# Kernel tuning notes

Measured on AMD Instinct MI355X. Metric: run time of the kernel, lower is better.

Reference implementation:

```python
import jax, jax.numpy as jnp
import numpy as np

N, B, FD, D, MSG, SCN, H, FFN = 2048, 16, 128, 32, 32, 16, 4, 64
HD = D // H


def _lin(k, o, i, scale=0.05):
    kw, kb = jax.random.split(k)
    return (jax.random.normal(kw, (o, i), jnp.float32) * scale,
            jax.random.normal(kb, (o,), jnp.float32) * scale)


def setup_inputs() -> dict:
    key = jax.random.key(0)
    ks = jax.random.split(key, 24)
    inp = {}
    inp['src'] = jax.random.randint(ks[0], (B,), 0, N)
    inp['dst'] = jax.random.randint(ks[1], (B,), 0, N)
    inp['edge_feat'] = jax.random.normal(ks[2], (B, 3), jnp.float32)
    inp['timestamps'] = jax.random.uniform(ks[3], (B,), dtype=jnp.float32)
    inp['node_features'] = jax.random.normal(ks[4], (N, FD), jnp.float32)
    inp['adj'] = jnp.zeros((N, N), jnp.float32)  # unused: assume_identity_adj=True
    inp['memory'] = jax.random.normal(ks[5], (N, D), jnp.float32) * 0.1
    inp['W_emb'], inp['b_emb'] = _lin(ks[6], D, FD)
    inp['Wqkv'], inp['bqkv'] = _lin(ks[7], 3 * D, D)
    inp['Wo'], inp['bo'] = _lin(ks[8], D, D)
    inp['g1'] = jnp.ones((D,), jnp.float32); inp['be1'] = jnp.zeros((D,), jnp.float32)
    inp['g2'] = jnp.ones((D,), jnp.float32); inp['be2'] = jnp.zeros((D,), jnp.float32)
    inp['W_f1'], inp['b_f1'] = _lin(ks[9], FFN, D)
    inp['W_f2'], inp['b_f2'] = _lin(ks[10], D, FFN)
    inp['W_scn'], inp['b_scn'] = _lin(ks[11], SCN, D)
    inp['g_scn'] = jnp.ones((SCN,), jnp.float32); inp['be_scn'] = jnp.zeros((SCN,), jnp.float32)
    inp['W_e1'], inp['b_e1'] = _lin(ks[12], 32, 2 * SCN)
    inp['W_e2'], inp['b_e2'] = _lin(ks[13], 16, 32)
    inp['W_e3'], inp['b_e3'] = _lin(ks[14], 1, 16)
    inp['gru_Wih'], inp['gru_bih'] = _lin(ks[15], 3 * D, MSG)
    inp['gru_Whh'], inp['gru_bhh'] = _lin(ks[16], 3 * D, D)
    inp['W_m1'], inp['b_m1'] = _lin(ks[17], MSG, 2 * D + 3)
    inp['W_m2'], inp['b_m2'] = _lin(ks[18], MSG, MSG)
    return inp


def _ln(x, g, b):
    mu = x.mean(-1, keepdims=True)
    var = ((x - mu) ** 2).mean(-1, keepdims=True)
    return (x - mu) * jax.lax.rsqrt(var + 1e-5) * g + b


def _gru(x, h, Wih, Whh, bih, bhh):
    # torch.nn.GRUCell semantics
    gi = x @ Wih.T + bih
    gh = h @ Whh.T + bhh
    ir, iz, i_n = jnp.split(gi, 3, -1)
    hr, hz, h_n = jnp.split(gh, 3, -1)
    r = jax.nn.sigmoid(ir + hr)
    z = jax.nn.sigmoid(iz + hz)
    n = jnp.tanh(i_n + r * h_n)
    return (1.0 - z) * n + z * h


def _update_memory(memory, src, dst, edge_feat,
                   gru_Wih, gru_Whh, gru_bih, gru_bhh, W_m1, b_m1, W_m2, b_m2):
    # messages computed from pre-update memory (as in torch source)
    msg_in = jnp.concatenate([memory[src], memory[dst], edge_feat], axis=1)  # [B, 2D+3]
    messages = jax.nn.relu(msg_in @ W_m1.T + b_m1) @ W_m2.T + b_m2           # [B, MSG]

    def step(mem, inp):
        s, d, m = inp
        hs = _gru(m, mem[s], gru_Wih, gru_Whh, gru_bih, gru_bhh)
        mem = mem.at[s].set(hs)
        hd = _gru(m, mem[d], gru_Wih, gru_Whh, gru_bih, gru_bhh)  # sees updated mem if d==s earlier
        mem = mem.at[d].set(hd)
        return mem, None

    new_mem, _ = jax.lax.scan(step, memory, (src, dst, messages))
    return new_mem


def _edge_logits(node_features, src, dst,
                 W_emb, b_emb, Wqkv, bqkv, Wo, bo, g1, be1, g2, be2,
                 W_f1, b_f1, W_f2, b_f2, W_scn, b_scn, g_scn, be_scn,
                 W_e1, b_e1, W_e2, b_e2, W_e3, b_e3):
    x0 = node_features @ W_emb.T + b_emb                      # [N, D]
    x = jnp.broadcast_to(x0[None], (B, N, D))                 # [B, N, D]
    # --- Graph transformer layer (MHA, eval mode: dropout = identity) ---
    qkv = x @ Wqkv.T + bqkv                                   # [B, N, 3D]
    q, k, v = jnp.split(qkv, 3, -1)
    q = q.reshape(B, N, H, HD)
    k = k.reshape(B, N, H, HD)
    v = v.reshape(B, N, H, HD)
    scores = jnp.einsum('bqhd,bkhd->bhqk', q, k) / np.sqrt(HD)
    attn = jax.nn.softmax(scores, axis=-1)
    ao = jnp.einsum('bhqk,bkhd->bqhd', attn, v).reshape(B, N, D)
    ao = ao @ Wo.T + bo
    x = _ln(x + ao, g1, be1)
    ffn = jax.nn.gelu(x @ W_f1.T + b_f1, approximate=False) @ W_f2.T + b_f2
    x = _ln(x + ffn, g2, be2)
    # --- SCN layer (identity adjacency assumed) ---
    s_out = jax.nn.relu(_ln(x @ W_scn.T + b_scn, g_scn, be_scn))  # [B, N, SCN]
    bi = jnp.arange(B)
    src_emb = s_out[bi, src]
    dst_emb = s_out[bi, dst]
    h = jnp.concatenate([src_emb, dst_emb], axis=-1)
    h = jax.nn.relu(h @ W_e1.T + b_e1)
    h = jax.nn.relu(h @ W_e2.T + b_e2)
    return (h @ W_e3.T + b_e3).squeeze(-1)                    # [B]


def reference(src, dst, edge_feat, timestamps, node_features, adj, memory,
              W_emb, b_emb, Wqkv, bqkv, Wo, bo, g1, be1, g2, be2,
              W_f1, b_f1, W_f2, b_f2, W_scn, b_scn, g_scn, be_scn,
              W_e1, b_e1, W_e2, b_e2, W_e3, b_e3,
              gru_Wih, gru_bih, gru_Whh, gru_bhh, W_m1, b_m1, W_m2, b_m2):
    new_mem = _update_memory(memory, src, dst, edge_feat,
                             gru_Wih, gru_Whh, gru_bih, gru_bhh,
                             W_m1, b_m1, W_m2, b_m2)
    edge_logit = _edge_logits(node_features, src, dst,
                              W_emb, b_emb, Wqkv, bqkv, Wo, bo, g1, be1, g2, be2,
                              W_f1, b_f1, W_f2, b_f2, W_scn, b_scn, g_scn, be_scn,
                              W_e1, b_e1, W_e2, b_e2, W_e3, b_e3)
    return edge_logit, new_mem
```

## Files before the change

kernel.cpp:

```cpp
#include <hip/hip_runtime.h>
#include <math.h>

#define NN   2048
#define BB   16

#define WS_X0   0
#define WS_QT   65536
#define WS_KT   131072
#define WS_VT   196608
#define WS_PART 262144
#define WS_GI   268800

__device__ __forceinline__ float sigmoidf_(float x) { return 1.0f / (1.0f + __expf(-x)); }
__device__ __forceinline__ float tanhf_(float x) {
    float ex = __expf(2.0f * x);
    return 1.0f - 2.0f / (ex + 1.0f);
}
__device__ __forceinline__ float dot4_(float4 a, float4 b) {
    return a.x*b.x + a.y*b.y + a.z*b.z + a.w*b.w;
}

__global__ __launch_bounds__(256) void k1_embed_qkv(
    const float* __restrict__ nf, const float* __restrict__ Wemb, const float* __restrict__ bemb,
    const float* __restrict__ Wqkv, const float* __restrict__ bqkv,
    const float* __restrict__ mem, const int* __restrict__ src, const int* __restrict__ dst,
    const float* __restrict__ ef,
    const float* __restrict__ Wm1, const float* __restrict__ bm1,
    const float* __restrict__ Wm2, const float* __restrict__ bm2,
    const float* __restrict__ Wih, const float* __restrict__ bih,
    float* __restrict__ ws, float* __restrict__ out)
{
    __shared__ float We_s[32 * 130];
    __shared__ float nf_s[8 * 130];
    __shared__ float x0_s[8 * 33];
    __shared__ float Wq_s[96 * 33];
    __shared__ __align__(16) float Wm1_s[32 * 67];
    __shared__ float Wm2_s[32 * 33];
    __shared__ float Wih_s[96 * 33];
    __shared__ float min_s[16 * 67];
    __shared__ float mr_s[16 * 33];
    __shared__ float msg_s[16 * 33];

    const int t = threadIdx.x, bx = blockIdx.x;

    if (bx == 256) {
        for (int idx = t; idx < 536; idx += 256)
            ((float4*)Wm1_s)[idx] = ((const float4*)Wm1)[idx];
        for (int idx = t; idx < 256; idx += 256) {
            float4 v = ((const float4*)Wm2)[idx];
            int o = idx >> 3, i = (idx & 7) * 4;
            Wm2_s[o * 33 + i] = v.x; Wm2_s[o * 33 + i + 1] = v.y;
            Wm2_s[o * 33 + i + 2] = v.z; Wm2_s[o * 33 + i + 3] = v.w;
        }
        for (int idx = t; idx < 768; idx += 256) {
            float4 v = ((const float4*)Wih)[idx];
            int o = idx >> 3, i = (idx & 7) * 4;
            Wih_s[o * 33 + i] = v.x; Wih_s[o * 33 + i + 1] = v.y;
            Wih_s[o * 33 + i + 2] = v.z; Wih_s[o * 33 + i + 3] = v.w;
        }
        for (int idx = t; idx < 16 * 67; idx += 256) {
            int e = idx / 67, i = idx - e * 67;
            float v;
            if (i < 32)      v = mem[src[e] * 32 + i];
            else if (i < 64) v = mem[dst[e] * 32 + (i - 32)];
            else             v = ef[e * 3 + (i - 64)];
            min_s[idx] = v;
        }
        __syncthreads();
        {
            int o = t & 31, e0 = t >> 5;
            for (int p = 0; p < 2; ++p) {
                int e = e0 + p * 8;
                float acc = bm1[o];
                for (int i = 0; i < 67; ++i) acc += Wm1_s[o * 67 + i] * min_s[e * 67 + i];
                mr_s[e * 33 + o] = fmaxf(acc, 0.f);
            }
        }
        __syncthreads();
        {
            int o = t & 31, e0 = t >> 5;
            for (int p = 0; p < 2; ++p) {
                int e = e0 + p * 8;
                float acc = bm2[o];
                #pragma unroll 8
                for (int i = 0; i < 32; ++i) acc += Wm2_s[o * 33 + i] * mr_s[e * 33 + i];
                msg_s[e * 33 + o] = acc;
            }
        }
        __syncthreads();
        {
            float* gi_g = ws + WS_GI;
            for (int idx = t; idx < 1536; idx += 256) {
                int e = idx / 96, o = idx - e * 96;
                float acc = bih[o];
                #pragma unroll 8
                for (int i = 0; i < 32; ++i) acc += Wih_s[o * 33 + i] * msg_s[e * 33 + i];
                gi_g[idx] = acc;
            }
        }
        return;
    }

    if (bx < 64) {
        int g = bx * 256 + t;
        ((float4*)(out + 16))[g] = ((const float4*)mem)[g];
    }

    const int j = t >> 5, o = t & 31;
    const int n = bx * 8 + j;

    for (int idx = t; idx < 1024; idx += 256) {
        float4 v = ((const float4*)Wemb)[idx];
        int r = idx >> 5, c = (idx & 31) * 4;
        We_s[r * 130 + c] = v.x; We_s[r * 130 + c + 1] = v.y;
        We_s[r * 130 + c + 2] = v.z; We_s[r * 130 + c + 3] = v.w;
    }
    for (int idx = t; idx < 768; idx += 256) {
        float4 v = ((const float4*)Wqkv)[idx];
        int r = idx >> 3, c = (idx & 7) * 4;
        Wq_s[r * 33 + c] = v.x; Wq_s[r * 33 + c + 1] = v.y;
        Wq_s[r * 33 + c + 2] = v.z; Wq_s[r * 33 + c + 3] = v.w;
    }
    for (int idx = t; idx < 256; idx += 256) {
        float4 v = ((const float4*)nf)[(bx * 8 + (idx >> 5)) * 32 + (idx & 31)];
        int r = idx >> 5, c = (idx & 31) * 4;
        nf_s[r * 130 + c] = v.x; nf_s[r * 130 + c + 1] = v.y;
        nf_s[r * 130 + c + 2] = v.z; nf_s[r * 130 + c + 3] = v.w;
    }
    __syncthreads();

    float acc = bemb[o];
    {
        const float2* Wr = (const float2*)&We_s[o * 130];
        const float2* Nr = (const float2*)&nf_s[j * 130];
        float sx = 0.f, sy = 0.f;
        #pragma unroll 16
        for (int i = 0; i < 64; ++i) {
            float2 w = Wr[i], x = Nr[i];
            sx += w.x * x.x; sy += w.y * x.y;
        }
        acc += sx + sy;
    }
    x0_s[j * 33 + o] = acc;
    ws[WS_X0 + n * 32 + o] = acc;
    __syncthreads();

    #pragma unroll
    for (int c = 0; c < 3; ++c) {
        int oo = c * 32 + o;
        float a2 = bqkv[oo];
        #pragma unroll 8
        for (int i = 0; i < 32; ++i) a2 += Wq_s[oo * 33 + i] * x0_s[j * 33 + i];
        int h = o >> 3, d = o & 7;
        float* base = ws + (c == 0 ? WS_QT : (c == 1 ? WS_KT : WS_VT));
        base[h * 16384 + n * 8 + d] = a2;
    }
}

__global__ __launch_bounds__(256) void k2_attn(
    const int* __restrict__ src, const int* __restrict__ dst,
    float* __restrict__ ws)
{
    const int t = threadIdx.x, bx = blockIdx.x;
    const int s  = bx >> 2;
    const int ks = bx & 3;
    const int h  = t >> 6;
    const int l  = t & 63;

    const int e = s >> 1;
    const int n = (s & 1) ? dst[e] : src[e];

    const float* qg = ws + WS_QT + h * 16384 + n * 8;
    const float4 qa  = *(const float4*)qg;
    const float4 qb4 = *(const float4*)(qg + 4);
    const float* kbase = ws + WS_KT + h * 16384;
    const float* vbase = ws + WS_VT + h * 16384;

    float4 oa = make_float4(0.f, 0.f, 0.f, 0.f);
    float4 ob = make_float4(0.f, 0.f, 0.f, 0.f);
    float ssum = 0.f;
    const float scale = 0.35355339059327373f;

    #pragma unroll
    for (int i = 0; i < 8; ++i) {
        const int key = ks * 512 + i * 64 + l;
        const float4 ka = *(const float4*)(kbase + key * 8);
        const float4 kb = *(const float4*)(kbase + key * 8 + 4);
        const float sc = (dot4_(qa, ka) + dot4_(qb4, kb)) * scale;
        const float p = __expf(sc);
        ssum += p;
        const float4 va = *(const float4*)(vbase + key * 8);
        const float4 vb = *(const float4*)(vbase + key * 8 + 4);
        oa.x += p * va.x; oa.y += p * va.y; oa.z += p * va.z; oa.w += p * va.w;
        ob.x += p * vb.x; ob.y += p * vb.y; ob.z += p * vb.z; ob.w += p * vb.w;
    }

    #pragma unroll
    for (int m = 1; m <= 32; m <<= 1) {
        ssum += __shfl_xor(ssum, m);
        oa.x += __shfl_xor(oa.x, m); oa.y += __shfl_xor(oa.y, m);
        oa.z += __shfl_xor(oa.z, m); oa.w += __shfl_xor(oa.w, m);
        ob.x += __shfl_xor(ob.x, m); ob.y += __shfl_xor(ob.y, m);
        ob.z += __shfl_xor(ob.z, m); ob.w += __shfl_xor(ob.w, m);
    }
    if (l == 0) {
        float* p = ws + WS_PART + ((s * 4 + h) * 4 + ks) * 12;
        *(float4*)p       = oa;
        *(float4*)(p + 4) = ob;
        p[8] = ssum;
    }
}

__global__ __launch_bounds__(1024) void k34_post_scan(
    const int* __restrict__ src, const int* __restrict__ dst,
    const float* __restrict__ mem,
    const float* __restrict__ Wo, const float* __restrict__ bo,
    const float* __restrict__ g1, const float* __restrict__ be1,
    const float* __restrict__ Wf1, const float* __restrict__ bf1,
    const float* __restrict__ Wf2, const float* __restrict__ bf2,
    const float* __restrict__ g2, const float* __restrict__ be2,
    const float* __restrict__ Wscn, const float* __restrict__ bscn,
    const float* __restrict__ gscn, const float* __restrict__ bescn,
    const float* __restrict__ Whh, const float* __restrict__ bhh,
    const float* __restrict__ We1, const float* __restrict__ be1e,
    const float* __restrict__ We2, const float* __restrict__ be2e,
    const float* __restrict__ We3, const float* __restrict__ be3,
    float* __restrict__ ws, float* __restrict__ out)
{
    __shared__ float Wo_s[32 * 33];
    __shared__ float Wf1_s[64 * 33];
    __shared__ float Wf2_s[32 * 65];
    __shared__ float Ws_s[16 * 33];
    __shared__ float arow[32 * 33];
    __shared__ float x1s[32 * 33];
    __shared__ float fs[32 * 65];
    __shared__ float sout_s[32 * 17];
    __shared__ float We1_s[32 * 33];
    __shared__ float We2_s[16 * 33];
    __shared__ float gi_s[16 * 97];
    __shared__ __align__(16) float slots[32 * 36];
    __shared__ int nid_s[32], fid_s[32], last_s[32];

    const int t = threadIdx.x;
    const int j = t >> 5, o = t & 31;

    float4 w1[8], w2[8], w3[8];
    float b1 = 0.f, b2 = 0.f, b3 = 0.f;
    if (t < 64) {
        const int r2 = (t < 32) ? t + 64 : t - 32;
        const int r3 = t + 32;
        #pragma unroll
        for (int c = 0; c < 8; ++c) {
            w1[c] = ((const float4*)Whh)[t * 8 + c];
            w2[c] = ((const float4*)Whh)[r2 * 8 + c];
            w3[c] = ((const float4*)Whh)[r3 * 8 + c];
        }
        b1 = bhh[t]; b2 = bhh[r2]; b3 = bhh[r3];
    }

    for (int idx = t; idx < 1024; idx += 1024) { int r = idx >> 5, c = idx & 31; Wo_s[r * 33 + c] = Wo[idx]; }
    for (int idx = t; idx < 2048; idx += 1024) { int r = idx >> 5, c = idx & 31; Wf1_s[r * 33 + c] = Wf1[idx]; }
    for (int idx = t; idx < 2048; idx += 1024) { int r = idx >> 6, c = idx & 63; Wf2_s[r * 65 + c] = Wf2[idx]; }
    for (int idx = t; idx < 512;  idx += 1024) { int r = idx >> 5, c = idx & 31; Ws_s[r * 33 + c] = Wscn[idx]; }
    for (int idx = t; idx < 1024; idx += 1024) { int r = idx >> 5, c = idx & 31; We1_s[r * 33 + c] = We1[idx]; }
    for (int idx = t; idx < 512;  idx += 1024) { int r = idx >> 5, c = idx & 31; We2_s[r * 33 + c] = We2[idx]; }
    for (int idx = t; idx < 1536; idx += 1024) { int e = idx / 96, oo = idx - e * 96; gi_s[e * 97 + oo] = ws[WS_GI + idx]; }
    if (t < 32) nid_s[t] = (t & 1) ? dst[t >> 1] : src[t >> 1];

    const int ej = j >> 1;
    const int n = (j & 1) ? dst[ej] : src[ej];
    {
        const int h = o >> 3, d = o & 7;
        float num = 0.f, den = 0.f;
        #pragma unroll
        for (int ks = 0; ks < 4; ++ks) {
            const float* p = ws + WS_PART + ((j * 4 + h) * 4 + ks) * 12;
            num += p[d];
            den += p[8];
        }
        arow[j * 33 + o] = num / den;
    }
    const float x0v = ws[WS_X0 + n * 32 + o];
    __syncthreads();

    if (t < 32) {
        int me = nid_s[t], f = t;
        for (int j2 = 0; j2 < t; ++j2) if (nid_s[j2] == me) { f = j2; break; }
        fid_s[t] = f;
        int isl = 1;
        for (int j2 = t + 1; j2 < 32; ++j2) if (nid_s[j2] == me) { isl = 0; break; }
        last_s[t] = isl;
    }
    float a = bo[o];
    #pragma unroll 8
    for (int i = 0; i < 32; ++i) a += Wo_s[o * 33 + i] * arow[j * 33 + i];
    float t1 = x0v + a;
    float mu = t1;
    #pragma unroll
    for (int m = 16; m >= 1; m >>= 1) mu += __shfl_xor(mu, m, 32);
    mu *= (1.f / 32.f);
    float dv = t1 - mu;
    float var = dv * dv;
    #pragma unroll
    for (int m = 16; m >= 1; m >>= 1) var += __shfl_xor(var, m, 32);
    var *= (1.f / 32.f);
    float x1 = dv * rsqrtf(var + 1e-5f) * g1[o] + be1[o];
    x1s[j * 33 + o] = x1;
    __syncthreads();

    if (t < 1024) {
        int j2 = t >> 5;
        if (fid_s[j2] == j2) slots[j2 * 36 + o] = mem[nid_s[j2] * 32 + o];
    }
    #pragma unroll
    for (int c = 0; c < 2; ++c) {
        int oo = c * 32 + o;
        float f = bf1[oo];
        #pragma unroll 8
        for (int i = 0; i < 32; ++i) f += Wf1_s[oo * 33 + i] * x1s[j * 33 + i];
        fs[j * 65 + oo] = 0.5f * f * (1.f + erff(f * 0.70710678118654752f));
    }
    __syncthreads();

    float f2 = bf2[o];
    #pragma unroll 8
    for (int i = 0; i < 64; ++i) f2 += Wf2_s[o * 65 + i] * fs[j * 65 + i];
    float t2 = x1 + f2;
    float mu2 = t2;
    #pragma unroll
    for (int m = 16; m >= 1; m >>= 1) mu2 += __shfl_xor(mu2, m, 32);
    mu2 *= (1.f / 32.f);
    float dv2 = t2 - mu2;
    float var2 = dv2 * dv2;
    #pragma unroll
    for (int m = 16; m >= 1; m >>= 1) var2 += __shfl_xor(var2, m, 32);
    var2 *= (1.f / 32.f);
    float x2 = dv2 * rsqrtf(var2 + 1e-5f) * g2[o] + be2[o];
    __syncthreads();
    x1s[j * 33 + o] = x2;
    __syncthreads();

    if (o < 16) {
        float sc = bscn[o];
        #pragma unroll 8
        for (int i = 0; i < 32; ++i) sc += Ws_s[o * 33 + i] * x1s[j * 33 + i];
        float m16 = sc;
        #pragma unroll
        for (int m = 8; m >= 1; m >>= 1) m16 += __shfl_xor(m16, m, 16);
        m16 *= (1.f / 16.f);
        float d16 = sc - m16;
        float v16 = d16 * d16;
        #pragma unroll
        for (int m = 8; m >= 1; m >>= 1) v16 += __shfl_xor(v16, m, 16);
        v16 *= (1.f / 16.f);
        float sv = d16 * rsqrtf(v16 + 1e-5f) * gscn[o] + bescn[o];
        sout_s[j * 17 + o] = fmaxf(sv, 0.f);
    }
    __syncthreads();

    if (t < 512) {
        int e = t >> 5, i = t & 31;
        arow[e * 33 + i] = (i < 16) ? sout_s[(2 * e) * 17 + i]
                                    : sout_s[(2 * e + 1) * 17 + (i - 16)];
    }
    __syncthreads();

    if (t < 512) {
        int e = t >> 5;
        float acc = be1e[o];
        #pragma unroll 8
        for (int i = 0; i < 32; ++i) acc += We1_s[o * 33 + i] * arow[e * 33 + i];
        fs[e * 33 + o] = fmaxf(acc, 0.f);
    }
    __syncthreads();

    if (t < 256) {
        int e = t >> 4, o2 = t & 15;
        float acc = be2e[o2];
        #pragma unroll 8
        for (int i = 0; i < 32; ++i) acc += We2_s[o2 * 33 + i] * fs[e * 33 + i];
        fs[600 + e * 17 + o2] = fmaxf(acc, 0.f);
    }
    __syncthreads();

    if (t < 16) {
        float acc = be3[0];
        #pragma unroll
        for (int i = 0; i < 16; ++i) acc += We3[i] * fs[600 + t * 17 + i];
        out[t] = acc;
    }
    __syncthreads();

    if (t < 64) {
        const bool lowhalf = (t < 32);
        for (int e = 0; e < 16; ++e) {
            const int js = 2 * e, jd = 2 * e + 1;
            const int ss = fid_s[js], sd = fid_s[jd];
            const bool same = (nid_s[js] == nid_s[jd]);
            const int npass = same ? 2 : 1;
            for (int pass = 0; pass < npass; ++pass) {
                const bool do_src = (!same) || (pass == 0);
                const bool do_dst = (!same) || (pass == 1);
                float acc1 = b1, acc2 = b2, acc3 = b3;
                #pragma unroll
                for (int c = 0; c < 8; ++c) {
                    const float4 hs4 = *(const float4*)&slots[ss * 36 + 4 * c];
                    const float4 hd4 = *(const float4*)&slots[sd * 36 + 4 * c];
                    acc1 += dot4_(w1[c], hs4);
                    const float4 hm = lowhalf ? hs4 : hd4;
                    acc2 += dot4_(w2[c], hm);
                    acc3 += dot4_(w3[c], hd4);
                }
                const float shv = __shfl_xor(lowhalf ? acc3 : acc1, 32);
                const float hr = lowhalf ? acc1 : acc2;
                const float hz = shv;
                const float hn = lowhalf ? acc2 : acc3;
                const float ir  = gi_s[e * 97 + o];
                const float iz  = gi_s[e * 97 + 32 + o];
                const float inn = gi_s[e * 97 + 64 + o];
                const float r = sigmoidf_(ir + hr);
                const float z = sigmoidf_(iz + hz);
                const float nn = tanhf_(inn + r * hn);
                const int slot = lowhalf ? ss : sd;
                const float hold = slots[slot * 36 + o];
                const float hnew = (1.f - z) * nn + z * hold;
                const bool wr = lowhalf ? do_src : do_dst;
                if (wr) slots[slot * 36 + o] = hnew;
                __threadfence_block();
            }
        }
    }
    __syncthreads();

    {
        int j2 = t >> 5;
        if (t < 1024 && last_s[j2]) out[16 + nid_s[j2] * 32 + o] = slots[fid_s[j2] * 36 + o];
    }
}

extern "C" void kernel_launch(void* const* d_in, const int* in_sizes, int n_in,
                              void* d_out, int out_size, void* d_ws, size_t ws_size,
                              hipStream_t stream)
{
    (void)in_sizes; (void)n_in; (void)out_size; (void)ws_size;
    const int*   src   = (const int*)d_in[0];
    const int*   dst   = (const int*)d_in[1];
    const float* ef    = (const float*)d_in[2];
    const float* nf    = (const float*)d_in[4];
    const float* mem   = (const float*)d_in[6];
    const float* Wemb  = (const float*)d_in[7];
    const float* bemb  = (const float*)d_in[8];
    const float* Wqkv  = (const float*)d_in[9];
    const float* bqkv  = (const float*)d_in[10];
    const float* Wo    = (const float*)d_in[11];
    const float* bo    = (const float*)d_in[12];
    const float* g1    = (const float*)d_in[13];
    const float* be1   = (const float*)d_in[14];
    const float* g2    = (const float*)d_in[15];
    const float* be2   = (const float*)d_in[16];
    const float* Wf1   = (const float*)d_in[17];
    const float* bf1   = (const float*)d_in[18];
    const float* Wf2   = (const float*)d_in[19];
    const float* bf2   = (const float*)d_in[20];
    const float* Wscn  = (const float*)d_in[21];
    const float* bscn  = (const float*)d_in[22];
    const float* gscn  = (const float*)d_in[23];
    const float* bescn = (const float*)d_in[24];
    const float* We1   = (const float*)d_in[25];
    const float* be1e  = (const float*)d_in[26];
    const float* We2   = (const float*)d_in[27];
    const float* be2e  = (const float*)d_in[28];
    const float* We3   = (const float*)d_in[29];
    const float* be3   = (const float*)d_in[30];
    const float* Wih   = (const float*)d_in[31];
    const float* bih   = (const float*)d_in[32];
    const float* Whh   = (const float*)d_in[33];
    const float* bhh   = (const float*)d_in[34];
    const float* Wm1   = (const float*)d_in[35];
    const float* bm1   = (const float*)d_in[36];
    const float* Wm2   = (const float*)d_in[37];
    const float* bm2   = (const float*)d_in[38];
    float* out = (float*)d_out;
    float* ws  = (float*)d_ws;

    hipLaunchKernelGGL(k1_embed_qkv, dim3(257), dim3(256), 0, stream,
        nf, Wemb, bemb, Wqkv, bqkv, mem, src, dst, ef, Wm1, bm1, Wm2, bm2, Wih, bih, ws, out);
    hipLaunchKernelGGL(k2_attn, dim3(128), dim3(256), 0, stream, src, dst, ws);
    hipLaunchKernelGGL(k34_post_scan, dim3(1), dim3(1024), 0, stream,
        src, dst, mem, Wo, bo, g1, be1, Wf1, bf1, Wf2, bf2, g2, be2,
        Wscn, bscn, gscn, bescn, Whh, bhh, We1, be1e, We2, be2e, We3, be3, ws, out);
}
```

Measured before the change: 203.2 us.

## Shrink post-scan block to 256 threads and batch weight loads into registers

The single-block post-scan kernel now runs with 256 threads instead of 1024. Each thread handles four rows through unrolled loops, and the weight staging now issues all vectorized global loads into registers up front before writing them to shared memory. The embed/QKV kernel and the memory-message block also prefetch their weights into registers before the shared-memory stores, so load latencies overlap. Going to fewer threads cuts barrier cost and wave count in the serial tail kernel, but each thread does more sequential work and uses more registers.

```diff
diff --git a/kernel.cpp b/kernel.cpp
--- a/kernel.cpp
+++ b/kernel.cpp
@@ -44,27 +44,46 @@
     const int t = threadIdx.x, bx = blockIdx.x;
 
     if (bx == 256) {
-        for (int idx = t; idx < 536; idx += 256)
-            ((float4*)Wm1_s)[idx] = ((const float4*)Wm1)[idx];
-        for (int idx = t; idx < 256; idx += 256) {
-            float4 v = ((const float4*)Wm2)[idx];
+        float4 rm1[3], rm2, rih[3];
+        float rmin[5];
+        #pragma unroll
+        for (int k = 0; k < 3; ++k) {
+            int idx = t + 256 * k;
+            rm1[k] = (idx < 536) ? ((const float4*)Wm1)[idx] : make_float4(0,0,0,0);
+        }
+        rm2 = ((const float4*)Wm2)[t];
+        #pragma unroll
+        for (int k = 0; k < 3; ++k) rih[k] = ((const float4*)Wih)[t + 256 * k];
+        #pragma unroll
+        for (int k = 0; k < 5; ++k) {
+            int idx = t + 256 * k;
+            rmin[k] = 0.f;
+            if (idx < 1072) {
+                int e = idx / 67, i = idx - e * 67;
+                if (i < 32)      rmin[k] = mem[src[e] * 32 + i];
+                else if (i < 64) rmin[k] = mem[dst[e] * 32 + (i - 32)];
+                else             rmin[k] = ef[e * 3 + (i - 64)];
+            }
+        }
+        #pragma unroll
+        for (int k = 0; k < 3; ++k) {
+            int idx = t + 256 * k;
+            if (idx < 536) ((float4*)Wm1_s)[idx] = rm1[k];
+        }
+        { int o = t >> 3, i = (t & 7) * 4;
+          Wm2_s[o * 33 + i] = rm2.x; Wm2_s[o * 33 + i + 1] = rm2.y;
+          Wm2_s[o * 33 + i + 2] = rm2.z; Wm2_s[o * 33 + i + 3] = rm2.w; }
+        #pragma unroll
+        for (int k = 0; k < 3; ++k) {
+            int idx = t + 256 * k;
             int o = idx >> 3, i = (idx & 7) * 4;
-            Wm2_s[o * 33 + i] = v.x; Wm2_s[o * 33 + i + 1] = v.y;
-            Wm2_s[o * 33 + i + 2] = v.z; Wm2_s[o * 33 + i + 3] = v.w;
-        }
-        for (int idx = t; idx < 768; idx += 256) {
-            float4 v = ((const float4*)Wih)[idx];
-            int o = idx >> 3, i = (idx & 7) * 4;
-            Wih_s[o * 33 + i] = v.x; Wih_s[o * 33 + i + 1] = v.y;
-            Wih_s[o * 33 + i + 2] = v.z; Wih_s[o * 33 + i + 3] = v.w;
-        }
-        for (int idx = t; idx < 16 * 67; idx += 256) {
-            int e = idx / 67, i = idx - e * 67;
-            float v;
-            if (i < 32)      v = mem[src[e] * 32 + i];
-            else if (i < 64) v = mem[dst[e] * 32 + (i - 32)];
-            else             v = ef[e * 3 + (i - 64)];
-            min_s[idx] = v;
+            Wih_s[o * 33 + i] = rih[k].x; Wih_s[o * 33 + i + 1] = rih[k].y;
+            Wih_s[o * 33 + i + 2] = rih[k].z; Wih_s[o * 33 + i + 3] = rih[k].w;
+        }
+        #pragma unroll
+        for (int k = 0; k < 5; ++k) {
+            int idx = t + 256 * k;
+            if (idx < 1072) min_s[idx] = rmin[k];
         }
         __syncthreads();
         {
@@ -101,33 +120,41 @@
         return;
     }
 
+    float4 rA[4], rB[3], rC;
+    #pragma unroll
+    for (int k = 0; k < 4; ++k) rA[k] = ((const float4*)Wemb)[t + 256 * k];
+    #pragma unroll
+    for (int k = 0; k < 3; ++k) rB[k] = ((const float4*)Wqkv)[t + 256 * k];
+    rC = ((const float4*)nf)[bx * 256 + t];
+
     if (bx < 64) {
         int g = bx * 256 + t;
         ((float4*)(out + 16))[g] = ((const float4*)mem)[g];
     }
 
+    #pragma unroll
+    for (int k = 0; k < 4; ++k) {
+        int idx = t + 256 * k;
+        int r = idx >> 5, c = (idx & 31) * 4;
+        We_s[r * 130 + c] = rA[k].x; We_s[r * 130 + c + 1] = rA[k].y;
+        We_s[r * 130 + c + 2] = rA[k].z; We_s[r * 130 + c + 3] = rA[k].w;
+    }
+    #pragma unroll
+    for (int k = 0; k < 3; ++k) {
+        int idx = t + 256 * k;
+        int r = idx >> 3, c = (idx & 7) * 4;
+        Wq_s[r * 33 + c] = rB[k].x; Wq_s[r * 33 + c + 1] = rB[k].y;
+        Wq_s[r * 33 + c + 2] = rB[k].z; Wq_s[r * 33 + c + 3] = rB[k].w;
+    }
+    {
+        int r = t >> 5, c = (t & 31) * 4;
+        nf_s[r * 130 + c] = rC.x; nf_s[r * 130 + c + 1] = rC.y;
+        nf_s[r * 130 + c + 2] = rC.z; nf_s[r * 130 + c + 3] = rC.w;
+    }
+    __syncthreads();
+
     const int j = t >> 5, o = t & 31;
     const int n = bx * 8 + j;
-
-    for (int idx = t; idx < 1024; idx += 256) {
-        float4 v = ((const float4*)Wemb)[idx];
-        int r = idx >> 5, c = (idx & 31) * 4;
-        We_s[r * 130 + c] = v.x; We_s[r * 130 + c + 1] = v.y;
-        We_s[r * 130 + c + 2] = v.z; We_s[r * 130 + c + 3] = v.w;
-    }
-    for (int idx = t; idx < 768; idx += 256) {
-        float4 v = ((const float4*)Wqkv)[idx];
-        int r = idx >> 3, c = (idx & 7) * 4;
-        Wq_s[r * 33 + c] = v.x; Wq_s[r * 33 + c + 1] = v.y;
-        Wq_s[r * 33 + c + 2] = v.z; Wq_s[r * 33 + c + 3] = v.w;
-    }
-    for (int idx = t; idx < 256; idx += 256) {
-        float4 v = ((const float4*)nf)[(bx * 8 + (idx >> 5)) * 32 + (idx & 31)];
-        int r = idx >> 5, c = (idx & 31) * 4;
-        nf_s[r * 130 + c] = v.x; nf_s[r * 130 + c + 1] = v.y;
-        nf_s[r * 130 + c + 2] = v.z; nf_s[r * 130 + c + 3] = v.w;
-    }
-    __syncthreads();
 
     float acc = bemb[o];
     {
@@ -211,7 +238,7 @@
     }
 }
 
-__global__ __launch_bounds__(1024) void k34_post_scan(
+__global__ __launch_bounds__(256, 1) void k34_post_scan(
     const int* __restrict__ src, const int* __restrict__ dst,
     const float* __restrict__ mem,
     const float* __restrict__ Wo, const float* __restrict__ bo,
@@ -242,7 +269,7 @@
     __shared__ int nid_s[32], fid_s[32], last_s[32];
 
     const int t = threadIdx.x;
-    const int j = t >> 5, o = t & 31;
+    const int j0 = t >> 5, o = t & 31;
 
     float4 w1[8], w2[8], w3[8];
     float b1 = 0.f, b2 = 0.f, b3 = 0.f;
@@ -258,29 +285,67 @@
         b1 = bhh[t]; b2 = bhh[r2]; b3 = bhh[r3];
     }
 
-    for (int idx = t; idx < 1024; idx += 1024) { int r = idx >> 5, c = idx & 31; Wo_s[r * 33 + c] = Wo[idx]; }
-    for (int idx = t; idx < 2048; idx += 1024) { int r = idx >> 5, c = idx & 31; Wf1_s[r * 33 + c] = Wf1[idx]; }
-    for (int idx = t; idx < 2048; idx += 1024) { int r = idx >> 6, c = idx & 63; Wf2_s[r * 65 + c] = Wf2[idx]; }
-    for (int idx = t; idx < 512;  idx += 1024) { int r = idx >> 5, c = idx & 31; Ws_s[r * 33 + c] = Wscn[idx]; }
-    for (int idx = t; idx < 1024; idx += 1024) { int r = idx >> 5, c = idx & 31; We1_s[r * 33 + c] = We1[idx]; }
-    for (int idx = t; idx < 512;  idx += 1024) { int r = idx >> 5, c = idx & 31; We2_s[r * 33 + c] = We2[idx]; }
-    for (int idx = t; idx < 1536; idx += 1024) { int e = idx / 96, oo = idx - e * 96; gi_s[e * 97 + oo] = ws[WS_GI + idx]; }
+    float4 rWo, rF1a, rF1b, rF2a, rF2b, rE1, rWs, rE2, rG0, rG1;
+    rWo  = ((const float4*)Wo)[t];
+    rF1a = ((const float4*)Wf1)[t]; rF1b = ((const float4*)Wf1)[t + 256];
+    rF2a = ((const float4*)Wf2)[t]; rF2b = ((const float4*)Wf2)[t + 256];
+    rE1  = ((const float4*)We1)[t];
+    rG0  = ((const float4*)(ws + WS_GI))[t];
+    if (t < 128) {
+        rWs = ((const float4*)Wscn)[t];
+        rE2 = ((const float4*)We2)[t];
+        rG1 = ((const float4*)(ws + WS_GI))[t + 256];
+    }
     if (t < 32) nid_s[t] = (t & 1) ? dst[t >> 1] : src[t >> 1];
 
-    const int ej = j >> 1;
-    const int n = (j & 1) ? dst[ej] : src[ej];
-    {
+    { int r = t >> 3, c = (t & 7) * 4;
+      Wo_s[r * 33 + c] = rWo.x; Wo_s[r * 33 + c + 1] = rWo.y;
+      Wo_s[r * 33 + c + 2] = rWo.z; Wo_s[r * 33 + c + 3] = rWo.w;
+      We1_s[r * 33 + c] = rE1.x; We1_s[r * 33 + c + 1] = rE1.y;
+      We1_s[r * 33 + c + 2] = rE1.z; We1_s[r * 33 + c + 3] = rE1.w; }
+    { int r = t >> 3, c = (t & 7) * 4;
+      Wf1_s[r * 33 + c] = rF1a.x; Wf1_s[r * 33 + c + 1] = rF1a.y;
+      Wf1_s[r * 33 + c + 2] = rF1a.z; Wf1_s[r * 33 + c + 3] = rF1a.w;
+      int r2 = (t + 256) >> 3, c2 = ((t + 256) & 7) * 4;
+      Wf1_s[r2 * 33 + c2] = rF1b.x; Wf1_s[r2 * 33 + c2 + 1] = rF1b.y;
+      Wf1_s[r2 * 33 + c2 + 2] = rF1b.z; Wf1_s[r2 * 33 + c2 + 3] = rF1b.w; }
+    { int r = t >> 4, c = (t & 15) * 4;
+      Wf2_s[r * 65 + c] = rF2a.x; Wf2_s[r * 65 + c + 1] = rF2a.y;
+      Wf2_s[r * 65 + c + 2] = rF2a.z; Wf2_s[r * 65 + c + 3] = rF2a.w;
+      int r2 = (t + 256) >> 4, c2 = ((t + 256) & 15) * 4;
+      Wf2_s[r2 * 65 + c2] = rF2b.x; Wf2_s[r2 * 65 + c2 + 1] = rF2b.y;
+      Wf2_s[r2 * 65 + c2 + 2] = rF2b.z; Wf2_s[r2 * 65 + c2 + 3] = rF2b.w; }
+    { int f = 4 * t, e = f / 96, off = f - e * 96;
+      gi_s[e * 97 + off] = rG0.x; gi_s[e * 97 + off + 1] = rG0.y;
+      gi_s[e * 97 + off + 2] = rG0.z; gi_s[e * 97 + off + 3] = rG0.w; }
+    if (t < 128) {
+        int r = t >> 3, c = (t & 7) * 4;
+        Ws_s[r * 33 + c] = rWs.x; Ws_s[r * 33 + c + 1] = rWs.y;
+        Ws_s[r * 33 + c + 2] = rWs.z; Ws_s[r * 33 + c + 3] = rWs.w;
+        We2_s[r * 33 + c] = rE2.x; We2_s[r * 33 + c + 1] = rE2.y;
+        We2_s[r * 33 + c + 2] = rE2.z; We2_s[r * 33 + c + 3] = rE2.w;
+        int f = 4 * (t + 256), e2 = f / 96, off = f - e2 * 96;
+        gi_s[e2 * 97 + off] = rG1.x; gi_s[e2 * 97 + off + 1] = rG1.y;
+        gi_s[e2 * 97 + off + 2] = rG1.z; gi_s[e2 * 97 + off + 3] = rG1.w;
+    }
+
+    float x0v[4];
+    #pragma unroll
+    for (int si = 0; si < 4; ++si) {
+        const int jj = si * 8 + j0;
+        const int ej = jj >> 1;
+        const int n = (jj & 1) ? dst[ej] : src[ej];
         const int h = o >> 3, d = o & 7;
         float num = 0.f, den = 0.f;
         #pragma unroll
         for (int ks = 0; ks < 4; ++ks) {
-            const float* p = ws + WS_PART + ((j * 4 + h) * 4 + ks) * 12;
+            const float* p = ws + WS_PART + ((jj * 4 + h) * 4 + ks) * 12;
             num += p[d];
             den += p[8];
         }
-        arow[j * 33 + o] = num / den;
-    }
-    const float x0v = ws[WS_X0 + n * 32 + o];
+        arow[jj * 33 + o] = num / den;
+        x0v[si] = ws[WS_X0 + n * 32 + o];
+    }
     __syncthreads();
 
     if (t < 32) {
@@ -291,82 +356,102 @@
         for (int j2 = t + 1; j2 < 32; ++j2) if (nid_s[j2] == me) { isl = 0; break; }
         last_s[t] = isl;
     }
-    float a = bo[o];
-    #pragma unroll 8
-    for (int i = 0; i < 32; ++i) a += Wo_s[o * 33 + i] * arow[j * 33 + i];
-    float t1 = x0v + a;
-    float mu = t1;
-    #pragma unroll
-    for (int m = 16; m >= 1; m >>= 1) mu += __shfl_xor(mu, m, 32);
-    mu *= (1.f / 32.f);
-    float dv = t1 - mu;
-    float var = dv * dv;
-    #pragma unroll
-    for (int m = 16; m >= 1; m >>= 1) var += __shfl_xor(var, m, 32);
-    var *= (1.f / 32.f);
-    float x1 = dv * rsqrtf(var + 1e-5f) * g1[o] + be1[o];
-    x1s[j * 33 + o] = x1;
-    __syncthreads();
-
-    if (t < 1024) {
-        int j2 = t >> 5;
+    __syncthreads();
+
+    #pragma unroll
+    for (int k = 0; k < 4; ++k) {
+        int j2 = j0 + 8 * k;
         if (fid_s[j2] == j2) slots[j2 * 36 + o] = mem[nid_s[j2] * 32 + o];
     }
-    #pragma unroll
-    for (int c = 0; c < 2; ++c) {
-        int oo = c * 32 + o;
-        float f = bf1[oo];
+
+    #pragma unroll
+    for (int si = 0; si < 4; ++si) {
+        const int jj = si * 8 + j0;
+        float a = bo[o];
         #pragma unroll 8
-        for (int i = 0; i < 32; ++i) f += Wf1_s[oo * 33 + i] * x1s[j * 33 + i];
-        fs[j * 65 + oo] = 0.5f * f * (1.f + erff(f * 0.70710678118654752f));
-    }
-    __syncthreads();
-
-    float f2 = bf2[o];
-    #pragma unroll 8
-    for (int i = 0; i < 64; ++i) f2 += Wf2_s[o * 65 + i] * fs[j * 65 + i];
-    float t2 = x1 + f2;
-    float mu2 = t2;
-    #pragma unroll
-    for (int m = 16; m >= 1; m >>= 1) mu2 += __shfl_xor(mu2, m, 32);
-    mu2 *= (1.f / 32.f);
-    float dv2 = t2 - mu2;
-    float var2 = dv2 * dv2;
-    #pragma unroll
-    for (int m = 16; m >= 1; m >>= 1) var2 += __shfl_xor(var2, m, 32);
-    var2 *= (1.f / 32.f);
-    float x2 = dv2 * rsqrtf(var2 + 1e-5f) * g2[o] + be2[o];
-    __syncthreads();
-    x1s[j * 33 + o] = x2;
+        for (int i = 0; i < 32; ++i) a += Wo_s[o * 33 + i] * arow[jj * 33 + i];
+        float t1 = x0v[si] + a;
+        float mu = t1;
+        #pragma unroll
+        for (int m = 16; m >= 1; m >>= 1) mu += __shfl_xor(mu, m, 32);
+        mu *= (1.f / 32.f);
+        float dv = t1 - mu;
+        float var = dv * dv;
+        #pragma unroll
+        for (int m = 16; m >= 1; m >>= 1) var += __shfl_xor(var, m, 32);
+        var *= (1.f / 32.f);
+        x1s[jj * 33 + o] = dv * rsqrtf(var + 1e-5f) * g1[o] + be1[o];
+    }
+    __syncthreads();
+
+    #pragma unroll
+    for (int si = 0; si < 4; ++si) {
+        const int jj = si * 8 + j0;
+        #pragma unroll
+        for (int c = 0; c < 2; ++c) {
+            int oo = c * 32 + o;
+            float f = bf1[oo];
+            #pragma unroll 8
+            for (int i = 0; i < 32; ++i) f += Wf1_s[oo * 33 + i] * x1s[jj * 33 + i];
+            fs[jj * 65 + oo] = 0.5f * f * (1.f + erff(f * 0.70710678118654752f));
+        }
+    }
+    __syncthreads();
+
+    #pragma unroll
+    for (int si = 0; si < 4; ++si) {
+        const int jj = si * 8 + j0;
+        float f2 = bf2[o];
+        #pragma unroll 8
+        for (int i = 0; i < 64; ++i) f2 += Wf2_s[o * 65 + i] * fs[jj * 65 + i];
+        float t2 = x1s[jj * 33 + o] + f2;
+        float mu2 = t2;
+        #pragma unroll
+        for (int m = 16; m >= 1; m >>= 1) mu2 += __shfl_xor(mu2, m, 32);
+        mu2 *= (1.f / 32.f);
+        float dv2 = t2 - mu2;
+        float var2 = dv2 * dv2;
+        #pragma unroll
+        for (int m = 16; m >= 1; m >>= 1) var2 += __shfl_xor(var2, m, 32);
+        var2 *= (1.f / 32.f);
+        x1s[jj * 33 + o] = dv2 * rsqrtf(var2 + 1e-5f) * g2[o] + be2[o];
+    }
     __syncthreads();
 
     if (o < 16) {
-        float sc = bscn[o];
-        #pragma unroll 8
-        for (int i = 0; i < 32; ++i) sc += Ws_s[o * 33 + i] * x1s[j * 33 + i];
-        float m16 = sc;
-        #pragma unroll
-        for (int m = 8; m >= 1; m >>= 1) m16 += __shfl_xor(m16, m, 16);
-        m16 *= (1.f / 16.f);
-        float d16 = sc - m16;
-        float v16 = d16 * d16;
-        #pragma unroll
-        for (int m = 8; m >= 1; m >>= 1) v16 += __shfl_xor(v16, m, 16);
-        v16 *= (1.f / 16.f);
-        float sv = d16 * rsqrtf(v16 + 1e-5f) * gscn[o] + bescn[o];
-        sout_s[j * 17 + o] = fmaxf(sv, 0.f);
-    }
-    __syncthreads();
-
-    if (t < 512) {
-        int e = t >> 5, i = t & 31;
+        #pragma unroll
+        for (int si = 0; si < 4; ++si) {
+            const int jj = si * 8 + j0;
+            float sc = bscn[o];
+            #pragma unroll 8
+            for (int i = 0; i < 32; ++i) sc += Ws_s[o * 33 + i] * x1s[jj * 33 + i];
+            float m16 = sc;
+            #pragma unroll
+            for (int m = 8; m >= 1; m >>= 1) m16 += __shfl_xor(m16, m, 16);
+            m16 *= (1.f / 16.f);
+            float d16 = sc - m16;
+            float v16 = d16 * d16;
+            #pragma unroll
+            for (int m = 8; m >= 1; m >>= 1) v16 += __shfl_xor(v16, m, 16);
+            v16 *= (1.f / 16.f);
+            float sv = d16 * rsqrtf(v16 + 1e-5f) * gscn[o] + bescn[o];
+            sout_s[jj * 17 + o] = fmaxf(sv, 0.f);
+        }
+    }
+    __syncthreads();
+
+    #pragma unroll
+    for (int k = 0; k < 2; ++k) {
+        int idx = t + 256 * k;
+        int e = idx >> 5, i = idx & 31;
         arow[e * 33 + i] = (i < 16) ? sout_s[(2 * e) * 17 + i]
                                     : sout_s[(2 * e + 1) * 17 + (i - 16)];
     }
     __syncthreads();
 
-    if (t < 512) {
-        int e = t >> 5;
+    #pragma unroll
+    for (int k = 0; k < 2; ++k) {
+        int e = j0 + 8 * k;
         float acc = be1e[o];
         #pragma unroll 8
         for (int i = 0; i < 32; ++i) acc += We1_s[o * 33 + i] * arow[e * 33 + i];
@@ -374,7 +459,7 @@
     }
     __syncthreads();
 
-    if (t < 256) {
+    {
         int e = t >> 4, o2 = t & 15;
         float acc = be2e[o2];
         #pragma unroll 8
@@ -432,9 +517,10 @@
     }
     __syncthreads();
 
-    {
-        int j2 = t >> 5;
-        if (t < 1024 && last_s[j2]) out[16 + nid_s[j2] * 32 + o] = slots[fid_s[j2] * 36 + o];
+    #pragma unroll
+    for (int k = 0; k < 4; ++k) {
+        int j2 = j0 + 8 * k;
+        if (last_s[j2]) out[16 + nid_s[j2] * 32 + o] = slots[fid_s[j2] * 36 + o];
     }
 }
 
@@ -486,7 +572,7 @@
     hipLaunchKernelGGL(k1_embed_qkv, dim3(257), dim3(256), 0, stream,
         nf, Wemb, bemb, Wqkv, bqkv, mem, src, dst, ef, Wm1, bm1, Wm2, bm2, Wih, bih, ws, out);
     hipLaunchKernelGGL(k2_attn, dim3(128), dim3(256), 0, stream, src, dst, ws);
-    hipLaunchKernelGGL(k34_post_scan, dim3(1), dim3(1024), 0, stream,
+    hipLaunchKernelGGL(k34_post_scan, dim3(1), dim3(256), 0, stream,
         src, dst, mem, Wo, bo, g1, be1, Wf1, bf1, Wf2, bf2, g2, be2,
         Wscn, bscn, gscn, bescn, Whh, bhh, We1, be1e, We2, be2e, We3, be3, ws, out);
 }
```

Measured after the change: 179.5 us. 1.13x faster.
